# Performance work log

Hardware: AMD Instinct MI355X
Metric: run time of the kernel (lower is better)

Reference implementation:

```python
import jax, jax.numpy as jnp
import numpy as np
from jax.scipy.special import logsumexp

B, T, D = 16, 512, 768
S, H, O = 4, 48, 48
EMISS_W = 0.5  # args.emiss_nn_weight


def setup_inputs() -> dict:
    key = jax.random.key(0)
    ks = jax.random.split(key, 6)
    emb = jax.random.normal(ks[0], (B, T, D), jnp.float32)
    # obs must be valid per-source distributions over n_obs (log is taken)
    obs = jax.nn.softmax(2.0 * jax.random.normal(ks[1], (B, T, S, O), jnp.float32), axis=-1)
    # default prior init: priors = 0.001, priors[0] = 1, param = log(priors)
    p = jnp.full((H,), 0.001, jnp.float32).at[0].set(1.0)
    state_priors = jnp.log(p)
    unnorm_trans = jax.random.normal(ks[2], (H, H), jnp.float32)
    unnorm_emiss = jnp.zeros((S, H, O), jnp.float32)
    # xavier_uniform with relu gain for the per-source emission Linears
    bound = np.sqrt(2.0) * np.sqrt(6.0 / (D + H * O))
    W_emiss = jax.random.uniform(ks[3], (S, H * O, D), jnp.float32, -bound, bound)
    b_emiss = jnp.zeros((S, H * O), jnp.float32)
    seq_lengths = jax.random.randint(ks[4], (B,), T // 2, T + 1).astype(jnp.int32)
    seq_lengths = seq_lengths.at[0].set(T)  # max length == T
    return dict(emb=emb, obs=obs, state_priors=state_priors, unnorm_trans=unnorm_trans,
                unnorm_emiss=unnorm_emiss, W_emiss=W_emiss, b_emiss=b_emiss,
                seq_lengths=seq_lengths)


def _lognorm(x):
    return x - logsumexp(x, axis=-1, keepdims=True)


def reference(emb, obs, state_priors, unnorm_trans, unnorm_emiss, W_emiss, b_emiss, seq_lengths):
    lp = jax.nn.log_softmax(state_priors)                 # [H]
    log_trans = jax.nn.log_softmax(unnorm_trans, axis=-1)  # [H,H] (constant over b,t)
    emiss = jax.nn.softmax(unnorm_emiss, axis=-1)          # [S,H,O]

    # neural emissions: per-source Linear(d_emb -> H*O), softmax over O
    logits = jnp.einsum('btd,sod->btso', emb, W_emiss) + b_emiss  # [B,T,S,H*O]
    nn_emiss = jax.nn.softmax(logits.reshape(B, T, S, H, O), axis=-1)
    # (nn_trans is computed by NeuralModule in the original but discarded)

    log_emiss = jnp.log((1.0 - EMISS_W) * emiss[None, None] + EMISS_W * nn_emiss)  # [B,T,S,H,O]
    # log_matmul over obs axis, then sum over sources -> [B,T,H]
    lep = logsumexp(log_emiss + jnp.log(obs)[:, :, :, None, :], axis=-1).sum(axis=2)

    # forward recursion (normalized each step)
    a0 = _lognorm(lp + lep[:, 0])                          # [B,H]

    def fstep(a_prev, lep_t):
        a = _lognorm(lep_t + logsumexp(a_prev[:, :, None] + log_trans[None], axis=1))
        return a, a

    _, alphas = jax.lax.scan(fstep, a0, jnp.swapaxes(lep[:, 1:], 0, 1))
    log_alpha = jnp.concatenate([a0[:, None], jnp.swapaxes(alphas, 0, 1)], axis=1)  # [B,T,H]

    # backward recursion: beta[t] = logsumexp_j(trans[i,j] + lep[t,j] + beta[t+1,j])
    bT = jnp.zeros((B, H), lep.dtype)

    def bstep(b_next, lep_t):
        b = logsumexp(log_trans[None] + (lep_t + b_next)[:, None, :], axis=2)
        return b, b

    _, betas = jax.lax.scan(bstep, bT, jnp.swapaxes(lep[:, :T - 1], 0, 1), reverse=True)
    log_beta = jnp.concatenate([jnp.swapaxes(betas, 0, 1), bT[:, None]], axis=1)  # [B,T,H]
    # per-example roll by (length - T) along time, as in the original
    log_beta = jax.vmap(lambda b, s: jnp.roll(b, s, axis=0))(log_beta, seq_lengths - T)

    log_gamma = _lognorm(log_alpha + log_beta)             # [B,T,H]

    # xi_t = trans + alpha[t-1] (outer-sum) (lep[t] + beta[t]),  t = 1..T-1
    xi = (log_trans[None, None]
          + log_alpha[:, :-1, :, None]
          + (lep[:, 1:] + log_beta[:, 1:])[:, :, None, :])  # [B,T-1,H,H]
    xi = xi - logsumexp(xi, axis=(-2, -1), keepdims=True)

    log_prior = jnp.mean(jnp.sum(jnp.exp(log_gamma[:, 0]) * lp, axis=-1))

    tran_terms = jnp.sum(jnp.exp(xi) * log_trans[None, None], axis=(-2, -1))  # [B,T-1]
    mask_tr = (jnp.arange(T - 1)[None] < (seq_lengths - 1)[:, None]).astype(lep.dtype)
    log_tran = jnp.mean(jnp.sum(tran_terms * mask_tr, axis=1))

    emis_terms = jnp.sum(jnp.exp(log_gamma) * lep, axis=-1)  # [B,T]
    mask_em = (jnp.arange(T)[None] < seq_lengths[:, None]).astype(lep.dtype)
    log_emis = jnp.mean(jnp.sum(emis_terms * mask_em, axis=1))

    return log_prior + log_tran + log_emis
```

## Files before the change

kernel.cpp:

```cpp
#include <hip/hip_runtime.h>
#include <math.h>

namespace {

constexpr int Bn = 16, Tn = 512, Dn = 768, Sn = 4, Hn = 48, On = 48;
constexpr int Mn = Bn * Tn;
constexpr int Gn = Sn * Hn;
constexpr int Nn = Gn * On;
constexpr float EMISS_W = 0.5f;

constexpr size_t OFF_LP   = 0;
constexpr size_t OFF_LT   = 64;
constexpr size_t OFF_PT   = OFF_LT + Hn*Hn;
constexpr size_t OFF_EM   = OFF_PT + Hn*Hn;
constexpr size_t OFF_LEPP = OFF_EM + (size_t)Sn*Hn*On;
constexpr size_t OFF_LA   = OFF_LEPP + (size_t)Mn*Gn;
constexpr size_t OFF_LB   = OFF_LA + (size_t)Mn*Hn;
constexpr size_t OFF_RED  = OFF_LB + (size_t)Mn*Hn;
constexpr size_t FLOATS_END = OFF_RED + (size_t)Mn;

typedef __attribute__((ext_vector_type(8))) short short8;
typedef __attribute__((ext_vector_type(4))) float f32x4;

__device__ inline float waveSum(float v){
#pragma unroll
  for (int o = 32; o; o >>= 1) v += __shfl_xor(v, o);
  return v;
}

__device__ inline unsigned short f2bf(float f){
  unsigned int u = __float_as_uint(f);
  u += 0x7FFFu + ((u >> 16) & 1u);
  return (unsigned short)(u >> 16);
}

__device__ inline void gload_lds16(const void* g, void* l){
  __builtin_amdgcn_global_load_lds(
      (const __attribute__((address_space(1))) void*)g,
      (__attribute__((address_space(3))) void*)l, 16, 0, 0);
}

__global__ void convprep_kernel(const float* __restrict__ srcA, unsigned short* __restrict__ dstA,
                                int n4a,
                                const float* __restrict__ srcB, unsigned short* __restrict__ dstB,
                                int n4b,
                                const float* __restrict__ sp, const float* __restrict__ ut,
                                const float* __restrict__ ue, float* __restrict__ ws,
                                int nconv){
  const int tid = threadIdx.x;
  if ((int)blockIdx.x == nconv){
    float m = -INFINITY;
    for (int h = 0; h < Hn; ++h) m = fmaxf(m, sp[h]);
    float s = 0.f;
    for (int h = 0; h < Hn; ++h) s += __expf(sp[h] - m);
    float lse = m + __logf(s);
    if (tid < Hn) ws[OFF_LP + tid] = sp[tid] - lse;
    if (tid < Hn){
      const float* row = ut + tid * Hn;
      float mm = -INFINITY;
      for (int j = 0; j < Hn; ++j) mm = fmaxf(mm, row[j]);
      float ss = 0.f;
      for (int j = 0; j < Hn; ++j) ss += __expf(row[j] - mm);
      float l = mm + __logf(ss);
      for (int j = 0; j < Hn; ++j){
        float v = row[j] - l;
        ws[OFF_LT + tid*Hn + j] = v;
        ws[OFF_PT + tid*Hn + j] = __expf(v);
      }
    }
    for (int r = tid; r < Sn*Hn; r += blockDim.x){
      const float* row = ue + (size_t)r * On;
      float mm = -INFINITY;
      for (int o = 0; o < On; ++o) mm = fmaxf(mm, row[o]);
      float ss = 0.f;
      for (int o = 0; o < On; ++o) ss += __expf(row[o] - mm);
      float inv = 1.f/ss;
      for (int o = 0; o < On; ++o) ws[OFF_EM + (size_t)r*On + o] = __expf(row[o]-mm)*inv;
    }
    return;
  }
  int i = blockIdx.x * blockDim.x + tid;
  const float* s2; unsigned short* d; int k;
  if (i < n4a){ s2 = srcA; d = dstA; k = i; }
  else { k = i - n4a; if (k >= n4b) return; s2 = srcB; d = dstB; }
  float4 v = ((const float4*)s2)[k];
  ushort4 r;
  r.x = f2bf(v.x); r.y = f2bf(v.y); r.z = f2bf(v.z); r.w = f2bf(v.w);
  ((ushort4*)d)[k] = r;
}

constexpr int BM = 128, BN = 192, BK = 64;
constexpr int NKT = Dn / BK;

__global__ __launch_bounds__(256, 2) void gemm_lep_kernel(
    const unsigned short* __restrict__ embB, const unsigned short* __restrict__ WB,
    const float* __restrict__ bm, const float* __restrict__ obs,
    float* __restrict__ ws){
  __shared__ __align__(16) char smem[81920];
  const int tid = threadIdx.x, lane = tid & 63, w = tid >> 6;
  const int bid = blockIdx.y * (Mn/BM) + blockIdx.x;
  const int xcd = bid & 7, j_loc = bid >> 3;
  const int xm = xcd & 3, xn = xcd >> 2;
  const int mloc = j_loc & 15, nloc = j_loc >> 4;
  const int m0 = (xm*16 + mloc) * BM;
  const int by = xn*24 + nloc;
  const int N0 = by * BN;
  const int wm = w & 1, wn = w >> 1;
  const int lm = lane & 15, q = lane >> 4;
  const int key = lm & 7;
  const int srow = lane >> 3, spc = lane & 7;
  const int aoff0 = (q ^ key) << 4;
  const int aoff1 = ((4 + q) ^ key) << 4;

  f32x4 acc[4][6];
#pragma unroll
  for (int i = 0; i < 4; ++i)
#pragma unroll
    for (int j = 0; j < 6; ++j) acc[i][j] = (f32x4){0.f,0.f,0.f,0.f};

  auto stageA = [&](int kt, int i){
    const int idx = w*4 + i;
    const int row = idx*8 + srow;
    const int lc  = spc ^ (row & 7);
    gload_lds16(embB + (size_t)(m0+row)*Dn + kt*BK + lc*8,
                smem + (kt & 1)*16384 + idx*1024);
  };
  auto stageB = [&](int kt, int i){
    const int idx = w*6 + i;
    const int row = idx*8 + srow;
    const int lc  = spc ^ (row & 7);
    gload_lds16(WB + (size_t)(N0+row)*Dn + kt*BK + lc*8,
                smem + 32768 + (kt & 1)*24576 + idx*1024);
  };

#pragma unroll
  for (int i = 0; i < 4; ++i) stageA(0, i);
#pragma unroll
  for (int i = 0; i < 6; ++i) stageB(0, i);

  for (int kt = 0; kt < NKT; ++kt){
    const char* Ab = smem + (kt & 1)*16384;
    const char* Bb = smem + 32768 + (kt & 1)*24576;

    asm volatile("s_waitcnt vmcnt(0)" ::: "memory");
    asm volatile("s_barrier" ::: "memory");

    short8 a0[4], a1[4], b0[3], b1[3], b2[3], b3[3];
#pragma unroll
    for (int j = 0; j < 3; ++j)
      b0[j] = *(const short8*)(Bb + (wn*96 + j*16 + lm)*128 + aoff0);
#pragma unroll
    for (int i = 0; i < 4; ++i)
      a0[i] = *(const short8*)(Ab + (wm*64 + i*16 + lm)*128 + aoff0);
#pragma unroll
    for (int j = 0; j < 3; ++j)
      b1[j] = *(const short8*)(Bb + (wn*96 + (3+j)*16 + lm)*128 + aoff0);
#pragma unroll
    for (int i = 0; i < 4; ++i)
      a1[i] = *(const short8*)(Ab + (wm*64 + i*16 + lm)*128 + aoff1);
#pragma unroll
    for (int j = 0; j < 3; ++j)
      b2[j] = *(const short8*)(Bb + (wn*96 + j*16 + lm)*128 + aoff1);
#pragma unroll
    for (int j = 0; j < 3; ++j)
      b3[j] = *(const short8*)(Bb + (wn*96 + (3+j)*16 + lm)*128 + aoff1);

    const int pf = kt + 1;
    if (pf < NKT){
#pragma unroll
      for (int i = 0; i < 4; ++i) stageA(pf, i);
#pragma unroll
      for (int i = 0; i < 6; ++i) stageB(pf, i);
    }

    __builtin_amdgcn_s_setprio(1);
#pragma unroll
    for (int i = 0; i < 4; ++i)
#pragma unroll
      for (int j = 0; j < 3; ++j)
        acc[i][j] = __builtin_amdgcn_mfma_f32_16x16x32_bf16(a0[i], b0[j], acc[i][j], 0, 0, 0);
#pragma unroll
    for (int i = 0; i < 4; ++i)
#pragma unroll
      for (int j = 0; j < 3; ++j)
        acc[i][3+j] = __builtin_amdgcn_mfma_f32_16x16x32_bf16(a0[i], b1[j], acc[i][3+j], 0, 0, 0);
#pragma unroll
    for (int i = 0; i < 4; ++i)
#pragma unroll
      for (int j = 0; j < 3; ++j)
        acc[i][j] = __builtin_amdgcn_mfma_f32_16x16x32_bf16(a1[i], b2[j], acc[i][j], 0, 0, 0);
#pragma unroll
    for (int i = 0; i < 4; ++i)
#pragma unroll
      for (int j = 0; j < 3; ++j)
        acc[i][3+j] = __builtin_amdgcn_mfma_f32_16x16x32_bf16(a1[i], b3[j], acc[i][3+j], 0, 0, 0);
    __builtin_amdgcn_s_setprio(0);
  }

  __syncthreads();
  float* Cp  = (float*)smem;
  float* ext = (float*)(smem + 49408);
  if (tid < 192){
    ext[tid]       = bm[N0 + tid];
    ext[192 + tid] = ws[OFF_EM + N0 + tid];
  }
#pragma unroll
  for (int h = 0; h < 2; ++h){
    if (h) __syncthreads();
    if (wm == h){
#pragma unroll
      for (int i = 0; i < 4; ++i)
#pragma unroll
        for (int j = 0; j < 6; ++j){
          const int col = wn*96 + j*16 + lm;
#pragma unroll
          for (int r = 0; r < 4; ++r){
            const int rowl = i*16 + q*4 + r;
            Cp[rowl*193 + col] = acc[i][j][r];
          }
        }
    }
    __syncthreads();
    {
      const int rowl = tid >> 2, grp = tid & 3;
      const int m = m0 + h*64 + rowl;
      const int g = by*4 + grp;
      const int s2 = g / Hn;
      const float* crow = Cp + rowl*193 + grp*48;
      const float* ob   = obs + ((size_t)m*Sn + s2)*On;
      const float* bi   = ext + grp*48;
      const float* em   = ext + 192 + grp*48;
      float Z = 0.f, pd = 0.f, eo = 0.f;
#pragma unroll
      for (int o = 0; o < On; ++o){
        float e = __expf(crow[o] + bi[o]);
        float obv = ob[o];
        Z += e;
        pd = fmaf(e, obv, pd);
        eo = fmaf(em[o], obv, eo);
      }
      ws[OFF_LEPP + (size_t)m*Gn + g] = __logf((1.f-EMISS_W)*eo + EMISS_W*(pd/Z));
    }
  }
}

constexpr int FBW = 24;
constexpr int FBL = 16;

__global__ __launch_bounds__(64) void fb_kernel(float* __restrict__ ws){
  __shared__ __align__(16) float ldsE[(FBW+FBL)*48];
  __shared__ __align__(16) float ring[2][64];
  const int lane = threadIdx.x;
  const int c    = blockIdx.x;
  const int b    = blockIdx.y;
  const bool fwd = blockIdx.z == 0;
  const bool act = lane < Hn;
  const int t0 = c*FBL, te = t0 + FBL - 1;

  float pt[Hn];
#pragma unroll
  for (int i = 0; i < Hn; ++i)
    pt[i] = act ? (fwd ? ws[OFF_PT + i*Hn + lane] : ws[OFF_PT + lane*Hn + i]) : 0.f;

  int row_lo, nrows, sA, sZ;
  bool exact;
  if (fwd){
    sA = t0 - FBW;
    exact = (sA < 1);
    row_lo = exact ? 0 : sA;
    if (exact) sA = 1;
    sZ = te;
    nrows = te - row_lo + 1;
  } else {
    int th = te + 1 + FBW;
    exact = (th > Tn - 2);
    sA = exact ? Tn - 2 : th - 1;
    sZ = t0;
    row_lo = t0;
    nrows = sA - t0 + 1;
  }

  {
    const float* src = ws + OFF_LEPP + ((size_t)b*Tn + row_lo)*Gn;
    int n4 = nrows * (Hn/4);
    for (int i = lane; i < n4; i += 64){
      int r = i / (Hn/4), h4 = i - r*(Hn/4);
      const float* p = src + (size_t)r*Gn + h4*4;
      float4 a = *(const float4*)(p);
      float4 b2 = *(const float4*)(p + Hn);
      float4 c2 = *(const float4*)(p + 2*Hn);
      float4 d2 = *(const float4*)(p + 3*Hn);
      float4 e;
      e.x = __expf(a.x + b2.x + c2.x + d2.x);
      e.y = __expf(a.y + b2.y + c2.y + d2.y);
      e.z = __expf(a.z + b2.z + c2.z + d2.z);
      e.w = __expf(a.w + b2.w + c2.w + d2.w);
      ((float4*)ldsE)[i] = e;
    }
  }
  __syncthreads();

  if (fwd){
    const size_t laF = OFF_LA + (size_t)b * Tn * Hn;
    float v;
    if (exact){
      v = act ? __expf(ws[OFF_LP + lane]) * ldsE[lane] : 0.f;
      if (c == 0 && act) ws[laF + lane] = v;
    } else {
      v = act ? 1.f : 0.f;
    }
    if (act) ring[0][lane] = v;
    __syncthreads();
    int cur = 0;
    for (int t = sA; t <= sZ; ++t){
      float S = waveSum(v);
      const float* rp = ring[cur];
      float s0=0.f,s1=0.f,s2=0.f,s3=0.f;
#pragma unroll
      for (int i = 0; i < Hn; i += 4){
        float4 a = *(const float4*)(rp + i);
        s0 = fmaf(a.x, pt[i+0], s0); s1 = fmaf(a.y, pt[i+1], s1);
        s2 = fmaf(a.z, pt[i+2], s2); s3 = fmaf(a.w, pt[i+3], s3);
      }
      float sd = (s0+s1)+(s2+s3);
      float e = act ? ldsE[(t - row_lo)*Hn + lane] : 0.f;
      float vn = act ? e * sd * (1.f/S) : 0.f;
      cur ^= 1;
      if (act) ring[cur][lane] = vn;
      __syncthreads();
      if (act && t >= t0) ws[laF + (size_t)t*Hn + lane] = vn;
      v = vn;
    }
  } else {
    const size_t lbF = OFF_LB + (size_t)b * Tn * Hn;
    float v = act ? 1.f : 0.f;
    if (exact && c == (Tn/FBL - 1) && act) ws[lbF + (size_t)(Tn-1)*Hn + lane] = 1.f;
    int cur = 0;
    for (int t = sA; t >= sZ; --t){
      float e = act ? ldsE[(t - row_lo)*Hn + lane] : 0.f;
      float wv = e * v;
      if (act) ring[cur][lane] = wv;
      float S = waveSum(wv);
      __syncthreads();
      const float* rp = ring[cur];
      float s0=0.f,s1=0.f,s2=0.f,s3=0.f;
#pragma unroll
      for (int j = 0; j < Hn; j += 4){
        float4 a = *(const float4*)(rp + j);
        s0 = fmaf(a.x, pt[j+0], s0); s1 = fmaf(a.y, pt[j+1], s1);
        s2 = fmaf(a.z, pt[j+2], s2); s3 = fmaf(a.w, pt[j+3], s3);
      }
      float vn = act ? ((s0+s1)+(s2+s3)) * (1.f/S) : 0.f;
      cur ^= 1;
      if (act && t <= te) ws[lbF + (size_t)t*Hn + lane] = vn;
      v = vn;
    }
  }
}

__global__ __launch_bounds__(256) void gamma_xi_kernel(
    const float* __restrict__ ws_c, float* __restrict__ ws,
    const int* __restrict__ seq_len){
  __shared__ float y_s[Hn], lap_s[Hn];
  __shared__ float red[8];
  const int tid = threadIdx.x;
  const int bid = blockIdx.x;
  const int b = bid >> 9, t = bid & (Tn-1);
  const int len = seq_len[b];
  int tb = t + (Tn - len); if (tb >= Tn) tb -= Tn;
  const size_t bt = (size_t)b*Tn + t;
  float lep = 0.f;
  if (tid < Hn){
    const float* lpp = ws_c + OFF_LEPP + bt*Gn + tid;
    lep = lpp[0] + lpp[Hn] + lpp[2*Hn] + lpp[3*Hn];
    float lb  = ws_c[OFF_LB + ((size_t)b*Tn + tb)*Hn + tid];
    y_s[tid] = __expf(lep) * lb;
    if (t >= 1) lap_s[tid] = ws_c[OFF_LA + (bt-1)*Hn + tid];
  }
  float emis_term = 0.f, prior_term = 0.f;
  if (tid < 64){
    int h = (tid < Hn) ? tid : 0;
    float la  = ws_c[OFF_LA + bt*Hn + h];
    float lb  = ws_c[OFF_LB + ((size_t)b*Tn + tb)*Hn + h];
    float lp  = ws_c[OFF_LP + h];
    float wgt = (tid < Hn) ? la*lb : 0.f;
    float Z = waveSum(wgt);
    float inv = 1.f / Z;
    emis_term  = waveSum(wgt * lep) * inv;
    prior_term = waveSum(wgt * lp) * inv;
  }
  __syncthreads();
  float tran_term = 0.f;
  if (t >= 1){
    float se = 0.f, st = 0.f;
#pragma unroll
    for (int k=0;k<9;++k){
      int e = tid + k*256;
      int i = e / Hn, j = e - i*Hn;
      float e2 = ws_c[OFF_PT + e] * lap_s[i] * y_s[j];
      se += e2;
      st = fmaf(e2, ws_c[OFF_LT + e], st);
    }
    se = waveSum(se);
    st = waveSum(st);
    const int wid = tid >> 6;
    if ((tid & 63) == 0){ red[wid] = se; red[4+wid] = st; }
    __syncthreads();
    if (tid == 0){
      float SE = red[0]+red[1]+red[2]+red[3];
      float ST = red[4]+red[5]+red[6]+red[7];
      tran_term = ST / SE;
    }
  }
  if (tid == 0){
    float tot = 0.f;
    if (t < len)            tot += emis_term;
    if (t == 0)             tot += prior_term;
    if (t >= 1 && t < len)  tot += tran_term;
    ws[OFF_RED + bid] = tot;
  }
}

__global__ __launch_bounds__(256) void sum_kernel(const float* __restrict__ ws,
                                                  float* __restrict__ out){
  __shared__ float red[4];
  const int tid = threadIdx.x;
  float s = 0.f;
  for (int i = tid; i < Mn; i += 256) s += ws[OFF_RED + i];
  s = waveSum(s);
  if ((tid & 63) == 0) red[tid >> 6] = s;
  __syncthreads();
  if (tid == 0) out[0] = (red[0]+red[1]+red[2]+red[3]) * (1.f / Bn);
}

}

extern "C" void kernel_launch(void* const* d_in, const int* in_sizes, int n_in,
                              void* d_out, int out_size, void* d_ws, size_t ws_size,
                              hipStream_t stream){
  const float* emb = (const float*)d_in[0];
  const float* obs = (const float*)d_in[1];
  const float* sp  = (const float*)d_in[2];
  const float* ut  = (const float*)d_in[3];
  const float* ue  = (const float*)d_in[4];
  const float* Wm  = (const float*)d_in[5];
  const float* bm  = (const float*)d_in[6];
  const int*   sl  = (const int*)d_in[7];
  float* ws  = (float*)d_ws;
  float* out = (float*)d_out;
  (void)in_sizes; (void)n_in; (void)ws_size; (void)out_size;

  unsigned short* embB = (unsigned short*)(ws + FLOATS_END);
  unsigned short* WB   = embB + (size_t)Mn * Dn;

  const int n4a = Mn*Dn/4, n4b = Nn*Dn/4;
  const int nconv = (n4a + n4b + 255)/256;
  convprep_kernel<<<nconv + 1, 256, 0, stream>>>(emb, embB, n4a, Wm, WB, n4b,
                                                 sp, ut, ue, ws, nconv);
  gemm_lep_kernel<<<dim3(Mn/BM, Nn/BN), 256, 0, stream>>>(embB, WB, bm, obs, ws);
  fb_kernel<<<dim3(Tn/FBL, Bn, 2), 64, 0, stream>>>(ws);
  gamma_xi_kernel<<<Bn*Tn, 256, 0, stream>>>(ws, ws, sl);
  sum_kernel<<<1, 256, 0, stream>>>(ws, out);
}
```

Measured before the change: 288.7 us.

## Load GEMM A operand directly into registers, keep only B in LDS

```diff
diff --git a/kernel.cpp b/kernel.cpp
--- a/kernel.cpp
+++ b/kernel.cpp
@@ -96,7 +96,7 @@
     const unsigned short* __restrict__ embB, const unsigned short* __restrict__ WB,
     const float* __restrict__ bm, const float* __restrict__ obs,
     float* __restrict__ ws){
-  __shared__ __align__(16) char smem[81920];
+  __shared__ __align__(16) char smem[51200];
   const int tid = threadIdx.x, lane = tid & 63, w = tid >> 6;
   const int bid = blockIdx.y * (Mn/BM) + blockIdx.x;
   const int xcd = bid & 7, j_loc = bid >> 3;
@@ -118,83 +118,71 @@
 #pragma unroll
     for (int j = 0; j < 6; ++j) acc[i][j] = (f32x4){0.f,0.f,0.f,0.f};
 
-  auto stageA = [&](int kt, int i){
-    const int idx = w*4 + i;
-    const int row = idx*8 + srow;
-    const int lc  = spc ^ (row & 7);
-    gload_lds16(embB + (size_t)(m0+row)*Dn + kt*BK + lc*8,
-                smem + (kt & 1)*16384 + idx*1024);
-  };
+  const unsigned short* aP[4];
+#pragma unroll
+  for (int mb = 0; mb < 4; ++mb)
+    aP[mb] = embB + (size_t)(m0 + wm*64 + mb*16 + lm)*Dn + q*8;
+
   auto stageB = [&](int kt, int i){
     const int idx = w*6 + i;
     const int row = idx*8 + srow;
     const int lc  = spc ^ (row & 7);
     gload_lds16(WB + (size_t)(N0+row)*Dn + kt*BK + lc*8,
-                smem + 32768 + (kt & 1)*24576 + idx*1024);
+                smem + (kt & 1)*24576 + idx*1024);
   };
 
-#pragma unroll
-  for (int i = 0; i < 4; ++i) stageA(0, i);
+  short8 aA[4][2], aB[4][2];
+
+#pragma unroll
+  for (int mb = 0; mb < 4; ++mb){
+    aA[mb][0] = *(const short8*)(aP[mb]);
+    aA[mb][1] = *(const short8*)(aP[mb] + 32);
+  }
+#pragma unroll
+  for (int mb = 0; mb < 4; ++mb) aP[mb] += BK;
 #pragma unroll
   for (int i = 0; i < 6; ++i) stageB(0, i);
 
-  for (int kt = 0; kt < NKT; ++kt){
-    const char* Ab = smem + (kt & 1)*16384;
-    const char* Bb = smem + 32768 + (kt & 1)*24576;
-
+  auto TILE = [&](int kt, short8 (&CUR)[4][2], short8 (&NXT)[4][2]){
     asm volatile("s_waitcnt vmcnt(0)" ::: "memory");
     asm volatile("s_barrier" ::: "memory");
-
-    short8 a0[4], a1[4], b0[3], b1[3], b2[3], b3[3];
-#pragma unroll
-    for (int j = 0; j < 3; ++j)
-      b0[j] = *(const short8*)(Bb + (wn*96 + j*16 + lm)*128 + aoff0);
-#pragma unroll
-    for (int i = 0; i < 4; ++i)
-      a0[i] = *(const short8*)(Ab + (wm*64 + i*16 + lm)*128 + aoff0);
-#pragma unroll
-    for (int j = 0; j < 3; ++j)
-      b1[j] = *(const short8*)(Bb + (wn*96 + (3+j)*16 + lm)*128 + aoff0);
-#pragma unroll
-    for (int i = 0; i < 4; ++i)
-      a1[i] = *(const short8*)(Ab + (wm*64 + i*16 + lm)*128 + aoff1);
-#pragma unroll
-    for (int j = 0; j < 3; ++j)
-      b2[j] = *(const short8*)(Bb + (wn*96 + j*16 + lm)*128 + aoff1);
-#pragma unroll
-    for (int j = 0; j < 3; ++j)
-      b3[j] = *(const short8*)(Bb + (wn*96 + (3+j)*16 + lm)*128 + aoff1);
-
     const int pf = kt + 1;
     if (pf < NKT){
 #pragma unroll
-      for (int i = 0; i < 4; ++i) stageA(pf, i);
+      for (int mb = 0; mb < 4; ++mb){
+        NXT[mb][0] = *(const short8*)(aP[mb]);
+        NXT[mb][1] = *(const short8*)(aP[mb] + 32);
+      }
+    }
+#pragma unroll
+    for (int mb = 0; mb < 4; ++mb) aP[mb] += BK;
+    const char* Bb = smem + (kt & 1)*24576;
+    short8 bf0[6], bf1[6];
+#pragma unroll
+    for (int j = 0; j < 6; ++j)
+      bf0[j] = *(const short8*)(Bb + (wn*96 + j*16 + lm)*128 + aoff0);
+#pragma unroll
+    for (int j = 0; j < 6; ++j)
+      bf1[j] = *(const short8*)(Bb + (wn*96 + j*16 + lm)*128 + aoff1);
+    if (pf < NKT){
 #pragma unroll
       for (int i = 0; i < 6; ++i) stageB(pf, i);
     }
-
-    __builtin_amdgcn_s_setprio(1);
 #pragma unroll
     for (int i = 0; i < 4; ++i)
 #pragma unroll
-      for (int j = 0; j < 3; ++j)
-        acc[i][j] = __builtin_amdgcn_mfma_f32_16x16x32_bf16(a0[i], b0[j], acc[i][j], 0, 0, 0);
+      for (int j = 0; j < 6; ++j)
+        acc[i][j] = __builtin_amdgcn_mfma_f32_16x16x32_bf16(CUR[i][0], bf0[j], acc[i][j], 0, 0, 0);
 #pragma unroll
     for (int i = 0; i < 4; ++i)
 #pragma unroll
-      for (int j = 0; j < 3; ++j)
-        acc[i][3+j] = __builtin_amdgcn_mfma_f32_16x16x32_bf16(a0[i], b1[j], acc[i][3+j], 0, 0, 0);
-#pragma unroll
-    for (int i = 0; i < 4; ++i)
-#pragma unroll
-      for (int j = 0; j < 3; ++j)
-        acc[i][j] = __builtin_amdgcn_mfma_f32_16x16x32_bf16(a1[i], b2[j], acc[i][j], 0, 0, 0);
-#pragma unroll
-    for (int i = 0; i < 4; ++i)
-#pragma unroll
-      for (int j = 0; j < 3; ++j)
-        acc[i][3+j] = __builtin_amdgcn_mfma_f32_16x16x32_bf16(a1[i], b3[j], acc[i][3+j], 0, 0, 0);
-    __builtin_amdgcn_s_setprio(0);
+      for (int j = 0; j < 6; ++j)
+        acc[i][j] = __builtin_amdgcn_mfma_f32_16x16x32_bf16(CUR[i][1], bf1[j], acc[i][j], 0, 0, 0);
+  };
+
+  for (int kt = 0; kt < NKT; kt += 2){
+    TILE(kt,     aA, aB);
+    TILE(kt + 1, aB, aA);
   }
 
   __syncthreads();
```

New measurement: 352.1 us. 22.0% more time.
